# Kernel tuning notes

Hardware: AMD Instinct MI355X
Metric: run time of the kernel (lower is better)

## Reference

```python
import jax, jax.numpy as jnp
import numpy as np

N = 500000       # total nodes
D = 256          # input_dim
H = 128          # hidden_dim
G = 4096         # number of graphs (batch.max()+1)


def setup_inputs() -> dict:
    key = jax.random.key(0)
    k_x, k_b, k_w1, k_b1, k_w2, k_b2 = jax.random.split(key, 6)
    x = jax.random.normal(k_x, (N, D), dtype=jnp.float32)
    batch = jnp.sort(jax.random.randint(k_b, (N,), 0, G)).astype(jnp.int64)
    batch = batch.at[-1].set(G - 1)  # ensure batch.max()+1 == G
    s1 = 1.0 / np.sqrt(D)
    s2 = 1.0 / np.sqrt(H)
    W1 = jax.random.uniform(k_w1, (D, H), jnp.float32, -s1, s1)
    b1 = jax.random.uniform(k_b1, (H,), jnp.float32, -s1, s1)
    W2 = jax.random.uniform(k_w2, (H, 1), jnp.float32, -s2, s2)
    b2 = jax.random.uniform(k_b2, (1,), jnp.float32, -s2, s2)
    return {"x": x, "batch": batch, "W1": W1, "b1": b1, "W2": W2, "b2": b2}


def reference(x, batch, W1, b1, W2, b2):
    # attention MLP: Linear -> Tanh -> Linear(->1)
    h = jnp.tanh(x @ W1 + b1)                  # [N, H]
    logits = (h @ W2 + b2)[:, 0]               # [N]
    # per-graph (segment) softmax over nodes
    m = jax.ops.segment_max(logits, batch, num_segments=G)       # [G]
    e = jnp.exp(logits - m[batch])                               # [N]
    denom = jax.ops.segment_sum(e, batch, num_segments=G)        # [G]
    w = e / denom[batch]                                         # [N]
    # weighted sum per graph; empty graphs -> zeros (matches torch branch)
    pooled = jax.ops.segment_sum(x * w[:, None], batch, num_segments=G)  # [G, D]
    return pooled
```

## Files before the change

kernel.cpp:

```cpp
#include <hip/hip_runtime.h>
#include <math.h>

#define D_DIM 256
#define H_DIM 128
#define TILE  32
#define HPAD  264

typedef __attribute__((ext_vector_type(8))) short bf16x8;
typedef __attribute__((ext_vector_type(4))) float f32x4;

__device__ __forceinline__ unsigned short f32_to_bf16(float f) {
  unsigned int u = __float_as_uint(f);
  u += 0x7FFFu + ((u >> 16) & 1u);
  return (unsigned short)(u >> 16);
}

__device__ __forceinline__ unsigned int pack_hi2(float f0, float f1, float& r0, float& r1) {
  unsigned int u0 = __float_as_uint(f0) & 0xFFFF0000u;
  unsigned int u1 = __float_as_uint(f1) & 0xFFFF0000u;
  r0 = f0 - __uint_as_float(u0);
  r1 = f1 - __uint_as_float(u1);
  return (u0 >> 16) | u1;
}
__device__ __forceinline__ unsigned int pack_lo2(float r0, float r1) {
  return (__float_as_uint(r0) >> 16) | (__float_as_uint(r1) & 0xFFFF0000u);
}

__device__ __forceinline__ float tanh_fast(float x) {
  float e = __expf(2.0f * x);
  return 1.0f - 2.0f / (e + 1.0f);
}

__global__ void setup_w1_kernel(const float* __restrict__ W1,
                                unsigned short* __restrict__ wfrag)
{
  const int t = threadIdx.x;
  const int l = t & 63, w = t >> 6;
  const int q = l >> 4, c = l & 15;
#pragma unroll
  for (int kt = 0; kt < 8; ++kt)
#pragma unroll
    for (int nt = 0; nt < 2; ++nt) {
      int f = kt * 2 + nt;
      int col = w * 32 + nt * 16 + c;
#pragma unroll
      for (int j = 0; j < 8; ++j) {
        int k = kt * 32 + q * 8 + j;
        wfrag[((size_t)f * 256 + t) * 8 + j] = f32_to_bf16(W1[k * H_DIM + col]);
      }
    }
}

__global__ void offsets_kernel(const void* __restrict__ batch, int* __restrict__ start,
                               int N, int G)
{
  int g = blockIdx.x * blockDim.x + threadIdx.x;
  if (g > G) return;
  const int* b32 = (const int*)batch;
  bool is64 = (b32[N - 1] != G - 1);
  int lo = 0, hi = N;
  while (lo < hi) {
    int mid = (lo + hi) >> 1;
    long long v = is64 ? ((const long long*)batch)[mid] : (long long)b32[mid];
    if (v < (long long)g) lo = mid + 1; else hi = mid;
  }
  start[g] = lo;
}

__device__ __forceinline__ void convert_store(unsigned short (*xh)[HPAD],
                                              unsigned short (*xl)[HPAD],
                                              int row, int col8, float4 A, float4 B)
{
  float r0, r1, r2, r3, r4, r5, r6, r7;
  uint4 H, L;
  H.x = pack_hi2(A.x, A.y, r0, r1);  H.y = pack_hi2(A.z, A.w, r2, r3);
  H.z = pack_hi2(B.x, B.y, r4, r5);  H.w = pack_hi2(B.z, B.w, r6, r7);
  L.x = pack_lo2(r0, r1);  L.y = pack_lo2(r2, r3);
  L.z = pack_lo2(r4, r5);  L.w = pack_lo2(r6, r7);
  *reinterpret_cast<uint4*>(&xh[row][col8]) = H;
  *reinterpret_cast<uint4*>(&xl[row][col8]) = L;
}

__global__ __launch_bounds__(256, 3)
void fused_kernel(const float* __restrict__ x, const unsigned short* __restrict__ wfrag,
                  const float* __restrict__ b1, const float* __restrict__ W2,
                  const int* __restrict__ start, float* __restrict__ out, int N)
{
  __shared__ unsigned short xhi[TILE][HPAD];
  __shared__ unsigned short xlo[TILE][HPAD];
  __shared__ float part[4][TILE];

  const int g = blockIdx.x;
  const int tid = threadIdx.x;
  const int s = start[g], e = start[g + 1];
  if (s >= e) { out[(size_t)g * D_DIM + tid] = 0.0f; return; }
  const int len = e - s;

  const int lane = tid & 63, w = tid >> 6;
  const int q = lane >> 4, c = lane & 15;
  const int srow = tid >> 5, scol8 = (tid & 31) * 8;

  bf16x8 wf[8][2];
#pragma unroll
  for (int kt = 0; kt < 8; ++kt)
#pragma unroll
    for (int nt = 0; nt < 2; ++nt)
      wf[kt][nt] = ((const bf16x8*)wfrag)[(kt * 2 + nt) * 256 + tid];

  float b1c[2], w2c[2];
#pragma unroll
  for (int nt = 0; nt < 2; ++nt) {
    int col = w * 32 + nt * 16 + c;
    b1c[nt] = b1[col];
    w2c[nt] = W2[col];
  }

  float m_run = -INFINITY, Z = 0.0f, accd = 0.0f;
  const int nT = (len + TILE - 1) / TILE;

  {
    const float4* g0 = reinterpret_cast<const float4*>(x + (size_t)min(s + srow,      N - 1) * D_DIM + scol8);
    const float4* g1 = reinterpret_cast<const float4*>(x + (size_t)min(s + srow +  8, N - 1) * D_DIM + scol8);
    const float4* g2 = reinterpret_cast<const float4*>(x + (size_t)min(s + srow + 16, N - 1) * D_DIM + scol8);
    const float4* g3 = reinterpret_cast<const float4*>(x + (size_t)min(s + srow + 24, N - 1) * D_DIM + scol8);
    convert_store(xhi, xlo, srow,      scol8, g0[0], g0[1]);
    convert_store(xhi, xlo, srow +  8, scol8, g1[0], g1[1]);
    convert_store(xhi, xlo, srow + 16, scol8, g2[0], g2[1]);
    convert_store(xhi, xlo, srow + 24, scol8, g3[0], g3[1]);
  }

  for (int ti = 0; ti < nT; ++ti) {
    const int t0 = ti * TILE;
    const int iend = min(TILE, len - t0);

    float4 pA0, pB0, pA1, pB1, pA2, pB2, pA3, pB3;
    {
      const int nb = s + t0 + TILE;
      const float4* g0 = reinterpret_cast<const float4*>(x + (size_t)min(nb + srow,      N - 1) * D_DIM + scol8);
      const float4* g1 = reinterpret_cast<const float4*>(x + (size_t)min(nb + srow +  8, N - 1) * D_DIM + scol8);
      const float4* g2 = reinterpret_cast<const float4*>(x + (size_t)min(nb + srow + 16, N - 1) * D_DIM + scol8);
      const float4* g3 = reinterpret_cast<const float4*>(x + (size_t)min(nb + srow + 24, N - 1) * D_DIM + scol8);
      pA0 = g0[0]; pB0 = g0[1];
      pA1 = g1[0]; pB1 = g1[1];
      pA2 = g2[0]; pB2 = g2[1];
      pA3 = g3[0]; pB3 = g3[1];
    }

    __syncthreads();

    f32x4 acc[2][2];
#pragma unroll
    for (int m = 0; m < 2; ++m)
#pragma unroll
      for (int nt = 0; nt < 2; ++nt) acc[m][nt] = (f32x4){0.f, 0.f, 0.f, 0.f};

#pragma unroll
    for (int kt = 0; kt < 8; ++kt) {
      const int koff = kt * 32 + q * 8;
      bf16x8 ah0 = *reinterpret_cast<const bf16x8*>(&xhi[c][koff]);
      bf16x8 al0 = *reinterpret_cast<const bf16x8*>(&xlo[c][koff]);
      bf16x8 ah1 = *reinterpret_cast<const bf16x8*>(&xhi[16 + c][koff]);
      bf16x8 al1 = *reinterpret_cast<const bf16x8*>(&xlo[16 + c][koff]);
#pragma unroll
      for (int nt = 0; nt < 2; ++nt) {
        acc[0][nt] = __builtin_amdgcn_mfma_f32_16x16x32_bf16(ah0, wf[kt][nt], acc[0][nt], 0, 0, 0);
        acc[0][nt] = __builtin_amdgcn_mfma_f32_16x16x32_bf16(al0, wf[kt][nt], acc[0][nt], 0, 0, 0);
        acc[1][nt] = __builtin_amdgcn_mfma_f32_16x16x32_bf16(ah1, wf[kt][nt], acc[1][nt], 0, 0, 0);
        acc[1][nt] = __builtin_amdgcn_mfma_f32_16x16x32_bf16(al1, wf[kt][nt], acc[1][nt], 0, 0, 0);
      }
    }

#pragma unroll
    for (int m = 0; m < 2; ++m)
#pragma unroll
      for (int r = 0; r < 4; ++r) {
        float v = tanh_fast(acc[m][0][r] + b1c[0]) * w2c[0]
                + tanh_fast(acc[m][1][r] + b1c[1]) * w2c[1];
#pragma unroll
        for (int o = 1; o < 16; o <<= 1) v += __shfl_xor(v, o, 64);
        if (c == 0) part[w][m * 16 + q * 4 + r] = v;
      }
    __syncthreads();

    {
      const int i = lane & 31;
      float li = (i < iend) ? (part[0][i] + part[1][i] + part[2][i] + part[3][i])
                            : -INFINITY;
      float tmax = li;
#pragma unroll
      for (int o = 1; o < 32; o <<= 1) tmax = fmaxf(tmax, __shfl_xor(tmax, o, 64));
      float m_new = fmaxf(m_run, tmax);
      float ei = __expf(li - m_new);
      float esum = ei;
#pragma unroll
      for (int o = 1; o < 32; o <<= 1) esum += __shfl_xor(esum, o, 64);
      float scale = __expf(m_run - m_new);
      Z = Z * scale + esum;

      float ac0 = 0.f, ac1 = 0.f, ac2 = 0.f, ac3 = 0.f;
#pragma unroll
      for (int ii = 0; ii < TILE; ii += 4) {
        float e0 = __shfl(ei, ii + 0, 64);
        float e1 = __shfl(ei, ii + 1, 64);
        float e2 = __shfl(ei, ii + 2, 64);
        float e3 = __shfl(ei, ii + 3, 64);
        float x0 = __uint_as_float((unsigned int)xhi[ii + 0][tid] << 16)
                 + __uint_as_float((unsigned int)xlo[ii + 0][tid] << 16);
        float x1 = __uint_as_float((unsigned int)xhi[ii + 1][tid] << 16)
                 + __uint_as_float((unsigned int)xlo[ii + 1][tid] << 16);
        float x2 = __uint_as_float((unsigned int)xhi[ii + 2][tid] << 16)
                 + __uint_as_float((unsigned int)xlo[ii + 2][tid] << 16);
        float x3 = __uint_as_float((unsigned int)xhi[ii + 3][tid] << 16)
                 + __uint_as_float((unsigned int)xlo[ii + 3][tid] << 16);
        ac0 = fmaf(e0, x0, ac0);
        ac1 = fmaf(e1, x1, ac1);
        ac2 = fmaf(e2, x2, ac2);
        ac3 = fmaf(e3, x3, ac3);
      }
      accd = fmaf(accd, scale, (ac0 + ac1) + (ac2 + ac3));
      m_run = m_new;
    }
    __syncthreads();

    convert_store(xhi, xlo, srow,      scol8, pA0, pB0);
    convert_store(xhi, xlo, srow +  8, scol8, pA1, pB1);
    convert_store(xhi, xlo, srow + 16, scol8, pA2, pB2);
    convert_store(xhi, xlo, srow + 24, scol8, pA3, pB3);
  }

  out[(size_t)g * D_DIM + tid] = accd / Z;
}

extern "C" void kernel_launch(void* const* d_in, const int* in_sizes, int n_in,
                              void* d_out, int out_size, void* d_ws, size_t ws_size,
                              hipStream_t stream)
{
  const float* x     = (const float*)d_in[0];
  const void*  batch = d_in[1];
  const float* W1    = (const float*)d_in[2];
  const float* b1    = (const float*)d_in[3];
  const float* W2    = (const float*)d_in[4];

  const int N = in_sizes[0] / D_DIM;
  const int G = out_size / D_DIM;

  unsigned short* wfrag = (unsigned short*)d_ws;
  int* startA = (int*)((char*)d_ws + 16 * 256 * 8 * sizeof(unsigned short));
  float* out = (float*)d_out;

  setup_w1_kernel<<<1, 256, 0, stream>>>(W1, wfrag);
  offsets_kernel<<<(G + 1 + 255) / 256, 256, 0, stream>>>(batch, startA, N, G);
  fused_kernel<<<G, 256, 0, stream>>>(x, wfrag, b1, W2, startA, out, N);
}
```

Measured before the change: 195.6 us.

## Drop low-bf16 MFMA pass, round hi part, and vectorize weighted pooling

The hi part of the split is now rounded to nearest instead of truncated, and the MFMA logits use only that part, which halves the matrix instructions and LDS fragment reads. The weighted pooling is restructured so each thread handles 4 rows by 8 dims using 128-bit LDS reads, followed by a final cross-slot reduction through a new LDS buffer. The per-tile logit partials are transposed so they can be read as one float4. This lowers the precision of the logits, since the lo correction is ignored in the MLP, and it adds LDS use and one more barrier at the end.

```diff
diff --git a/kernel.cpp b/kernel.cpp
--- a/kernel.cpp
+++ b/kernel.cpp
@@ -16,8 +16,8 @@
 }
 
 __device__ __forceinline__ unsigned int pack_hi2(float f0, float f1, float& r0, float& r1) {
-  unsigned int u0 = __float_as_uint(f0) & 0xFFFF0000u;
-  unsigned int u1 = __float_as_uint(f1) & 0xFFFF0000u;
+  unsigned int u0 = (__float_as_uint(f0) + 0x8000u) & 0xFFFF0000u;
+  unsigned int u1 = (__float_as_uint(f1) + 0x8000u) & 0xFFFF0000u;
   r0 = f0 - __uint_as_float(u0);
   r1 = f1 - __uint_as_float(u1);
   return (u0 >> 16) | u1;
@@ -88,7 +88,8 @@
 {
   __shared__ unsigned short xhi[TILE][HPAD];
   __shared__ unsigned short xlo[TILE][HPAD];
-  __shared__ float part[4][TILE];
+  __shared__ float part_t[TILE][4];
+  __shared__ float pacc_lds[8][D_DIM];
 
   const int g = blockIdx.x;
   const int tid = threadIdx.x;
@@ -99,6 +100,8 @@
   const int lane = tid & 63, w = tid >> 6;
   const int q = lane >> 4, c = lane & 15;
   const int srow = tid >> 5, scol8 = (tid & 31) * 8;
+  const int prow0 = w * 8 + (lane >> 5) * 4;
+  const int pdim  = (lane & 31) * 8;
 
   bf16x8 wf[8][2];
 #pragma unroll
@@ -115,7 +118,8 @@
     w2c[nt] = W2[col];
   }
 
-  float m_run = -INFINITY, Z = 0.0f, accd = 0.0f;
+  float m_run = -INFINITY, Z = 0.0f;
+  float pacc[8] = {0.f, 0.f, 0.f, 0.f, 0.f, 0.f, 0.f, 0.f};
   const int nT = (len + TILE - 1) / TILE;
 
   {
@@ -158,15 +162,11 @@
     for (int kt = 0; kt < 8; ++kt) {
       const int koff = kt * 32 + q * 8;
       bf16x8 ah0 = *reinterpret_cast<const bf16x8*>(&xhi[c][koff]);
-      bf16x8 al0 = *reinterpret_cast<const bf16x8*>(&xlo[c][koff]);
       bf16x8 ah1 = *reinterpret_cast<const bf16x8*>(&xhi[16 + c][koff]);
-      bf16x8 al1 = *reinterpret_cast<const bf16x8*>(&xlo[16 + c][koff]);
 #pragma unroll
       for (int nt = 0; nt < 2; ++nt) {
         acc[0][nt] = __builtin_amdgcn_mfma_f32_16x16x32_bf16(ah0, wf[kt][nt], acc[0][nt], 0, 0, 0);
-        acc[0][nt] = __builtin_amdgcn_mfma_f32_16x16x32_bf16(al0, wf[kt][nt], acc[0][nt], 0, 0, 0);
         acc[1][nt] = __builtin_amdgcn_mfma_f32_16x16x32_bf16(ah1, wf[kt][nt], acc[1][nt], 0, 0, 0);
-        acc[1][nt] = __builtin_amdgcn_mfma_f32_16x16x32_bf16(al1, wf[kt][nt], acc[1][nt], 0, 0, 0);
       }
     }
 
@@ -178,14 +178,14 @@
                 + tanh_fast(acc[m][1][r] + b1c[1]) * w2c[1];
 #pragma unroll
         for (int o = 1; o < 16; o <<= 1) v += __shfl_xor(v, o, 64);
-        if (c == 0) part[w][m * 16 + q * 4 + r] = v;
+        if (c == 0) part_t[m * 16 + q * 4 + r][w] = v;
       }
     __syncthreads();
 
     {
       const int i = lane & 31;
-      float li = (i < iend) ? (part[0][i] + part[1][i] + part[2][i] + part[3][i])
-                            : -INFINITY;
+      float4 pp = *reinterpret_cast<const float4*>(&part_t[i][0]);
+      float li = (i < iend) ? (pp.x + pp.y + pp.z + pp.w) : -INFINITY;
       float tmax = li;
 #pragma unroll
       for (int o = 1; o < 32; o <<= 1) tmax = fmaxf(tmax, __shfl_xor(tmax, o, 64));
@@ -196,29 +196,33 @@
       for (int o = 1; o < 32; o <<= 1) esum += __shfl_xor(esum, o, 64);
       float scale = __expf(m_run - m_new);
       Z = Z * scale + esum;
-
-      float ac0 = 0.f, ac1 = 0.f, ac2 = 0.f, ac3 = 0.f;
-#pragma unroll
-      for (int ii = 0; ii < TILE; ii += 4) {
-        float e0 = __shfl(ei, ii + 0, 64);
-        float e1 = __shfl(ei, ii + 1, 64);
-        float e2 = __shfl(ei, ii + 2, 64);
-        float e3 = __shfl(ei, ii + 3, 64);
-        float x0 = __uint_as_float((unsigned int)xhi[ii + 0][tid] << 16)
-                 + __uint_as_float((unsigned int)xlo[ii + 0][tid] << 16);
-        float x1 = __uint_as_float((unsigned int)xhi[ii + 1][tid] << 16)
-                 + __uint_as_float((unsigned int)xlo[ii + 1][tid] << 16);
-        float x2 = __uint_as_float((unsigned int)xhi[ii + 2][tid] << 16)
-                 + __uint_as_float((unsigned int)xlo[ii + 2][tid] << 16);
-        float x3 = __uint_as_float((unsigned int)xhi[ii + 3][tid] << 16)
-                 + __uint_as_float((unsigned int)xlo[ii + 3][tid] << 16);
-        ac0 = fmaf(e0, x0, ac0);
-        ac1 = fmaf(e1, x1, ac1);
-        ac2 = fmaf(e2, x2, ac2);
-        ac3 = fmaf(e3, x3, ac3);
-      }
-      accd = fmaf(accd, scale, (ac0 + ac1) + (ac2 + ac3));
       m_run = m_new;
+
+#pragma unroll
+      for (int j = 0; j < 8; ++j) pacc[j] *= scale;
+#pragma unroll
+      for (int rr = 0; rr < 4; ++rr) {
+        const int row = prow0 + rr;
+        float er = __shfl(ei, row, 64);
+        uint4 H = *reinterpret_cast<const uint4*>(&xhi[row][pdim]);
+        uint4 L = *reinterpret_cast<const uint4*>(&xlo[row][pdim]);
+        float x0 = __uint_as_float(H.x << 16)        + __uint_as_float(L.x << 16);
+        float x1 = __uint_as_float(H.x & 0xFFFF0000u) + __uint_as_float(L.x & 0xFFFF0000u);
+        float x2 = __uint_as_float(H.y << 16)        + __uint_as_float(L.y << 16);
+        float x3 = __uint_as_float(H.y & 0xFFFF0000u) + __uint_as_float(L.y & 0xFFFF0000u);
+        float x4 = __uint_as_float(H.z << 16)        + __uint_as_float(L.z << 16);
+        float x5 = __uint_as_float(H.z & 0xFFFF0000u) + __uint_as_float(L.z & 0xFFFF0000u);
+        float x6 = __uint_as_float(H.w << 16)        + __uint_as_float(L.w << 16);
+        float x7 = __uint_as_float(H.w & 0xFFFF0000u) + __uint_as_float(L.w & 0xFFFF0000u);
+        pacc[0] = fmaf(er, x0, pacc[0]);
+        pacc[1] = fmaf(er, x1, pacc[1]);
+        pacc[2] = fmaf(er, x2, pacc[2]);
+        pacc[3] = fmaf(er, x3, pacc[3]);
+        pacc[4] = fmaf(er, x4, pacc[4]);
+        pacc[5] = fmaf(er, x5, pacc[5]);
+        pacc[6] = fmaf(er, x6, pacc[6]);
+        pacc[7] = fmaf(er, x7, pacc[7]);
+      }
     }
     __syncthreads();
 
@@ -228,7 +232,18 @@
     convert_store(xhi, xlo, srow + 24, scol8, pA3, pB3);
   }
 
-  out[(size_t)g * D_DIM + tid] = accd / Z;
+  {
+    const int slot = w * 2 + (lane >> 5);
+    *reinterpret_cast<float4*>(&pacc_lds[slot][pdim])     =
+        make_float4(pacc[0], pacc[1], pacc[2], pacc[3]);
+    *reinterpret_cast<float4*>(&pacc_lds[slot][pdim + 4]) =
+        make_float4(pacc[4], pacc[5], pacc[6], pacc[7]);
+  }
+  __syncthreads();
+  float sum = 0.f;
+#pragma unroll
+  for (int r = 0; r < 8; ++r) sum += pacc_lds[r][tid];
+  out[(size_t)g * D_DIM + tid] = sum / Z;
 }
 
 extern "C" void kernel_launch(void* const* d_in, const int* in_sizes, int n_in,
```

New measurement: 293.0 us. 1.5x slower.

## Drop lo-part MFMA for logits, stream W1 fragments, split pooling by row halves

Applied to the files above, without the earlier changes.

The attention-logit GEMM now uses only the high bf16 part of x, halving MFMA work, and the high part is now rounded rather than truncated to limit the lost precision. W1 fragments are loaded from global memory inside the k-loop instead of being held in registers, which frees registers at the cost of repeated reads. The weighted pooling now has each thread cover two dimensions over half the rows using packed 32-bit LDS reads, and the two partial sums are combined in shared memory at the end. The logits lose precision and may drift from the reference.

```diff
diff --git a/kernel.cpp b/kernel.cpp
--- a/kernel.cpp
+++ b/kernel.cpp
@@ -16,8 +16,8 @@
 }
 
 __device__ __forceinline__ unsigned int pack_hi2(float f0, float f1, float& r0, float& r1) {
-  unsigned int u0 = __float_as_uint(f0) & 0xFFFF0000u;
-  unsigned int u1 = __float_as_uint(f1) & 0xFFFF0000u;
+  unsigned int u0 = (__float_as_uint(f0) + 0x8000u) & 0xFFFF0000u;
+  unsigned int u1 = (__float_as_uint(f1) + 0x8000u) & 0xFFFF0000u;
   r0 = f0 - __uint_as_float(u0);
   r1 = f1 - __uint_as_float(u1);
   return (u0 >> 16) | u1;
@@ -89,6 +89,7 @@
   __shared__ unsigned short xhi[TILE][HPAD];
   __shared__ unsigned short xlo[TILE][HPAD];
   __shared__ float part[4][TILE];
+  __shared__ float redbuf[2][D_DIM];
 
   const int g = blockIdx.x;
   const int tid = threadIdx.x;
@@ -99,23 +100,20 @@
   const int lane = tid & 63, w = tid >> 6;
   const int q = lane >> 4, c = lane & 15;
   const int srow = tid >> 5, scol8 = (tid & 31) * 8;
-
-  bf16x8 wf[8][2];
-#pragma unroll
-  for (int kt = 0; kt < 8; ++kt)
-#pragma unroll
-    for (int nt = 0; nt < 2; ++nt)
-      wf[kt][nt] = ((const bf16x8*)wfrag)[(kt * 2 + nt) * 256 + tid];
-
-  float b1c[2], w2c[2];
-#pragma unroll
-  for (int nt = 0; nt < 2; ++nt) {
-    int col = w * 32 + nt * 16 + c;
-    b1c[nt] = b1[col];
-    w2c[nt] = W2[col];
-  }
-
-  float m_run = -INFINITY, Z = 0.0f, accd = 0.0f;
+  const int halfsel = tid >> 7;
+  const int dim2 = (tid & 127) * 2;
+
+  const bf16x8* wfv = (const bf16x8*)wfrag;
+
+  float b1c0, b1c1, w2c0, w2c1;
+  {
+    int col0 = w * 32 + c, col1 = w * 32 + 16 + c;
+    b1c0 = b1[col0]; b1c1 = b1[col1];
+    w2c0 = W2[col0]; w2c1 = W2[col1];
+  }
+
+  float m_run = -INFINITY, Z = 0.0f;
+  float pcA = 0.f, pcB = 0.f;
   const int nT = (len + TILE - 1) / TILE;
 
   {
@@ -132,6 +130,8 @@
   for (int ti = 0; ti < nT; ++ti) {
     const int t0 = ti * TILE;
     const int iend = min(TILE, len - t0);
+
+    __syncthreads();
 
     float4 pA0, pB0, pA1, pB1, pA2, pB2, pA3, pB3;
     {
@@ -146,40 +146,35 @@
       pA3 = g3[0]; pB3 = g3[1];
     }
 
-    __syncthreads();
-
-    f32x4 acc[2][2];
-#pragma unroll
-    for (int m = 0; m < 2; ++m)
-#pragma unroll
-      for (int nt = 0; nt < 2; ++nt) acc[m][nt] = (f32x4){0.f, 0.f, 0.f, 0.f};
-
+    f32x4 acc00 = {0.f, 0.f, 0.f, 0.f}, acc01 = {0.f, 0.f, 0.f, 0.f};
+    f32x4 acc10 = {0.f, 0.f, 0.f, 0.f}, acc11 = {0.f, 0.f, 0.f, 0.f};
 #pragma unroll
     for (int kt = 0; kt < 8; ++kt) {
       const int koff = kt * 32 + q * 8;
       bf16x8 ah0 = *reinterpret_cast<const bf16x8*>(&xhi[c][koff]);
-      bf16x8 al0 = *reinterpret_cast<const bf16x8*>(&xlo[c][koff]);
       bf16x8 ah1 = *reinterpret_cast<const bf16x8*>(&xhi[16 + c][koff]);
-      bf16x8 al1 = *reinterpret_cast<const bf16x8*>(&xlo[16 + c][koff]);
-#pragma unroll
-      for (int nt = 0; nt < 2; ++nt) {
-        acc[0][nt] = __builtin_amdgcn_mfma_f32_16x16x32_bf16(ah0, wf[kt][nt], acc[0][nt], 0, 0, 0);
-        acc[0][nt] = __builtin_amdgcn_mfma_f32_16x16x32_bf16(al0, wf[kt][nt], acc[0][nt], 0, 0, 0);
-        acc[1][nt] = __builtin_amdgcn_mfma_f32_16x16x32_bf16(ah1, wf[kt][nt], acc[1][nt], 0, 0, 0);
-        acc[1][nt] = __builtin_amdgcn_mfma_f32_16x16x32_bf16(al1, wf[kt][nt], acc[1][nt], 0, 0, 0);
-      }
-    }
-
-#pragma unroll
-    for (int m = 0; m < 2; ++m)
-#pragma unroll
-      for (int r = 0; r < 4; ++r) {
-        float v = tanh_fast(acc[m][0][r] + b1c[0]) * w2c[0]
-                + tanh_fast(acc[m][1][r] + b1c[1]) * w2c[1];
-#pragma unroll
-        for (int o = 1; o < 16; o <<= 1) v += __shfl_xor(v, o, 64);
-        if (c == 0) part[w][m * 16 + q * 4 + r] = v;
-      }
+      bf16x8 bf0 = wfv[(kt * 2 + 0) * 256 + tid];
+      bf16x8 bf1 = wfv[(kt * 2 + 1) * 256 + tid];
+      acc00 = __builtin_amdgcn_mfma_f32_16x16x32_bf16(ah0, bf0, acc00, 0, 0, 0);
+      acc01 = __builtin_amdgcn_mfma_f32_16x16x32_bf16(ah0, bf1, acc01, 0, 0, 0);
+      acc10 = __builtin_amdgcn_mfma_f32_16x16x32_bf16(ah1, bf0, acc10, 0, 0, 0);
+      acc11 = __builtin_amdgcn_mfma_f32_16x16x32_bf16(ah1, bf1, acc11, 0, 0, 0);
+    }
+
+#pragma unroll
+    for (int r = 0; r < 4; ++r) {
+      float v = tanh_fast(acc00[r] + b1c0) * w2c0 + tanh_fast(acc01[r] + b1c1) * w2c1;
+#pragma unroll
+      for (int o = 1; o < 16; o <<= 1) v += __shfl_xor(v, o, 64);
+      if (c == 0) part[w][q * 4 + r] = v;
+    }
+#pragma unroll
+    for (int r = 0; r < 4; ++r) {
+      float v = tanh_fast(acc10[r] + b1c0) * w2c0 + tanh_fast(acc11[r] + b1c1) * w2c1;
+#pragma unroll
+      for (int o = 1; o < 16; o <<= 1) v += __shfl_xor(v, o, 64);
+      if (c == 0) part[w][16 + q * 4 + r] = v;
+    }
     __syncthreads();
 
     {
@@ -196,29 +191,20 @@
       for (int o = 1; o < 32; o <<= 1) esum += __shfl_xor(esum, o, 64);
       float scale = __expf(m_run - m_new);
       Z = Z * scale + esum;
-
-      float ac0 = 0.f, ac1 = 0.f, ac2 = 0.f, ac3 = 0.f;
-#pragma unroll
-      for (int ii = 0; ii < TILE; ii += 4) {
-        float e0 = __shfl(ei, ii + 0, 64);
-        float e1 = __shfl(ei, ii + 1, 64);
-        float e2 = __shfl(ei, ii + 2, 64);
-        float e3 = __shfl(ei, ii + 3, 64);
-        float x0 = __uint_as_float((unsigned int)xhi[ii + 0][tid] << 16)
-                 + __uint_as_float((unsigned int)xlo[ii + 0][tid] << 16);
-        float x1 = __uint_as_float((unsigned int)xhi[ii + 1][tid] << 16)
-                 + __uint_as_float((unsigned int)xlo[ii + 1][tid] << 16);
-        float x2 = __uint_as_float((unsigned int)xhi[ii + 2][tid] << 16)
-                 + __uint_as_float((unsigned int)xlo[ii + 2][tid] << 16);
-        float x3 = __uint_as_float((unsigned int)xhi[ii + 3][tid] << 16)
-                 + __uint_as_float((unsigned int)xlo[ii + 3][tid] << 16);
-        ac0 = fmaf(e0, x0, ac0);
-        ac1 = fmaf(e1, x1, ac1);
-        ac2 = fmaf(e2, x2, ac2);
-        ac3 = fmaf(e3, x3, ac3);
+      m_run = m_new;
+
+      pcA *= scale; pcB *= scale;
+#pragma unroll
+      for (int ii = 0; ii < 16; ++ii) {
+        const int row = halfsel * 16 + ii;
+        float er = __shfl(ei, row, 64);
+        unsigned int hx = *reinterpret_cast<const unsigned int*>(&xhi[row][dim2]);
+        unsigned int lx = *reinterpret_cast<const unsigned int*>(&xlo[row][dim2]);
+        float x0 = __uint_as_float(hx << 16)         + __uint_as_float(lx << 16);
+        float x1 = __uint_as_float(hx & 0xFFFF0000u) + __uint_as_float(lx & 0xFFFF0000u);
+        pcA = fmaf(er, x0, pcA);
+        pcB = fmaf(er, x1, pcB);
       }
-      accd = fmaf(accd, scale, (ac0 + ac1) + (ac2 + ac3));
-      m_run = m_new;
     }
     __syncthreads();
 
@@ -228,7 +214,10 @@
     convert_store(xhi, xlo, srow + 24, scol8, pA3, pB3);
   }
 
-  out[(size_t)g * D_DIM + tid] = accd / Z;
+  redbuf[halfsel][dim2]     = pcA;
+  redbuf[halfsel][dim2 + 1] = pcB;
+  __syncthreads();
+  out[(size_t)g * D_DIM + tid] = (redbuf[0][tid] + redbuf[1][tid]) / Z;
 }
 
 extern "C" void kernel_launch(void* const* d_in, const int* in_sizes, int n_in,
```

Result: slower. 222.4 us (+13.7%).
